# Performance work log

Measured on AMD Instinct MI355X. Metric: run time of the kernel, lower is better.

The kernel has to match this reference:

```python
import jax, jax.numpy as jnp
import numpy as np

B, E, IN, OUT = 512, 8, 1024, 1024


def setup_inputs() -> dict:
    key = jax.random.key(0)
    k1, k2, k3, k4 = jax.random.split(key, 4)
    x = jax.random.normal(k1, (B, IN), dtype=jnp.float32)
    expert_weights = jax.random.uniform(k2, (B, E), dtype=jnp.float32)
    # kaiming_uniform per expert with a=sqrt(5): bound = sqrt(6/((1+a^2)*fan_in)) = 1/sqrt(fan_in)
    wb = 1.0 / np.sqrt(IN)
    weight = jax.random.uniform(k3, (E, OUT, IN), dtype=jnp.float32, minval=-wb, maxval=wb)
    bias = jax.random.uniform(k4, (E, OUT), dtype=jnp.float32, minval=-wb, maxval=wb)
    return {"x": x, "expert_weights": expert_weights, "weight": weight, "bias": bias}


def reference(x, expert_weights, weight, bias):
    # Same math as: blended_W = einsum('bk,koi->boi'); bmm(blended_W, x[...,None]) + blended_b
    # fused as a single contraction to avoid the [B, out, in] intermediate.
    y = jnp.einsum('bk,koi,bi->bo', expert_weights, weight, x)
    b = jnp.einsum('bk,ko->bo', expert_weights, bias)
    return y + b
```

## Files before the change

### kernel.cpp

```cpp
#include <hip/hip_runtime.h>
#include <hip/hip_bf16.h>


#define BDIM 512
#define EDIM 8
#define INDIM 1024
#define OUTDIM 1024
#define NDIM (EDIM * OUTDIM)

typedef __attribute__((ext_vector_type(8))) short frag8;
typedef __attribute__((ext_vector_type(4))) float f32x4;

__device__ inline void async_ld16(void* lds, const void* g) {
  __builtin_amdgcn_global_load_lds(
      (const __attribute__((address_space(1))) void*)g,
      (__attribute__((address_space(3))) void*)lds, 16, 0, 0);
}

__device__ inline ushort f2bf(float f) {
  unsigned u = __builtin_bit_cast(unsigned, f);
  u += 0x7fffu + ((u >> 16) & 1u);
  return (ushort)(u >> 16);
}

__global__ __launch_bounds__(256) void prep_kernel(
    const float* __restrict__ W, const float* __restrict__ x,
    ushort* __restrict__ wsW, ushort* __restrict__ wsX) {
  const int NW = EDIM * OUTDIM * INDIM / 4;
  int i = blockIdx.x * 256 + threadIdx.x;
  const float4* src;
  ushort* dst;
  if (i < NW) {
    src = (const float4*)W + i;
    dst = wsW + (size_t)i * 4;
  } else {
    int j = i - NW;
    src = (const float4*)x + j;
    dst = wsX + (size_t)j * 4;
  }
  float4 v = *src;
  ushort4 o;
  o.x = f2bf(v.x); o.y = f2bf(v.y); o.z = f2bf(v.z); o.w = f2bf(v.w);
  *(ushort4*)dst = o;
}

#define TM 128
#define TN 128
#define BK 64

__global__ __launch_bounds__(256) void gemm_bt(
    const ushort* __restrict__ A,
    const ushort* __restrict__ Bm,
    float* __restrict__ Z) {
  __shared__ __align__(16) ushort As[TM * BK];
  __shared__ __align__(16) ushort Bs[TN * BK];

  const int tid  = threadIdx.x;
  const int lane = tid & 63;
  const int wave = tid >> 6;
  const int n0 = blockIdx.x * TN;
  const int m0 = blockIdx.y * TM;

  const int wr   = (wave >> 1) * 64;
  const int wc   = (wave & 1) * 64;
  const int l15  = lane & 15;
  const int quad = lane >> 4;

  const int srow  = lane >> 3;
  const int selem = (lane & 7) * 8;

  f32x4 acc[4][4] = {};

  for (int k0 = 0; k0 < INDIM; k0 += BK) {
#pragma unroll
    for (int c = 0; c < 4; ++c) {
      const int chunk = wave * 4 + c;
      const int row = chunk * 8 + srow;
      async_ld16(&As[chunk * 512],
                 A + (size_t)(m0 + row) * INDIM + k0 + selem);
      async_ld16(&Bs[chunk * 512],
                 Bm + (size_t)(n0 + row) * INDIM + k0 + selem);
    }
    __syncthreads();

#pragma unroll
    for (int kk = 0; kk < BK; kk += 32) {
      frag8 a[4], b[4];
#pragma unroll
      for (int i = 0; i < 4; ++i) {
        a[i] = *(const frag8*)&As[(wr + i * 16 + l15) * BK + kk + quad * 8];
        b[i] = *(const frag8*)&Bs[(wc + i * 16 + l15) * BK + kk + quad * 8];
      }
#pragma unroll
      for (int i = 0; i < 4; ++i)
#pragma unroll
        for (int j = 0; j < 4; ++j)
          acc[i][j] = __builtin_amdgcn_mfma_f32_16x16x32_bf16(a[i], b[j], acc[i][j], 0, 0, 0);
    }
    __syncthreads();
  }

#pragma unroll
  for (int i = 0; i < 4; ++i) {
    const int mrow = m0 + wr + i * 16 + quad * 4;
#pragma unroll
    for (int j = 0; j < 4; ++j) {
      const int ncol = n0 + wc + j * 16 + l15;
#pragma unroll
      for (int r = 0; r < 4; ++r)
        Z[(size_t)(mrow + r) * NDIM + ncol] = acc[i][j][r];
    }
  }
}

__global__ __launch_bounds__(256) void blend_kernel(
    const float* __restrict__ Z, const float* __restrict__ ew,
    const float* __restrict__ bias, float* __restrict__ out) {
  int idx = blockIdx.x * 256 + threadIdx.x;
  int b = idx >> 10;
  int o = idx & 1023;
  const float* zb = Z + (size_t)b * NDIM + o;
  float y = 0.f;
#pragma unroll
  for (int k = 0; k < EDIM; ++k)
    y += ew[b * EDIM + k] * (zb[k * OUTDIM] + bias[k * OUTDIM + o]);
  out[idx] = y;
}

__global__ __launch_bounds__(256) void fallback_kernel(
    const float* __restrict__ x, const float* __restrict__ ew,
    const float* __restrict__ W, const float* __restrict__ bias,
    float* __restrict__ out) {
  int idx = blockIdx.x * 256 + threadIdx.x;
  int b = idx >> 10;
  int o = idx & 1023;
  float y = 0.f;
  for (int k = 0; k < EDIM; ++k) {
    const float* wr = W + ((size_t)k * OUTDIM + o) * INDIM;
    const float* xr = x + (size_t)b * INDIM;
    float dot = 0.f;
    for (int i = 0; i < INDIM; ++i) dot += wr[i] * xr[i];
    y += ew[b * EDIM + k] * (dot + bias[k * OUTDIM + o]);
  }
  out[idx] = y;
}

extern "C" void kernel_launch(void* const* d_in, const int* in_sizes, int n_in,
                              void* d_out, int out_size, void* d_ws, size_t ws_size,
                              hipStream_t stream) {
  const float* x    = (const float*)d_in[0];
  const float* ew   = (const float*)d_in[1];
  const float* W    = (const float*)d_in[2];
  const float* bias = (const float*)d_in[3];
  float* out = (float*)d_out;

  const size_t offW = 0;
  const size_t offX = (size_t)16 << 20;
  const size_t offZ = (size_t)17 << 20;
  const size_t need = (size_t)33 << 20;

  if (ws_size < need) {
    fallback_kernel<<<2048, 256, 0, stream>>>(x, ew, W, bias, out);
    return;
  }

  char* ws = (char*)d_ws;
  ushort* wsW = (ushort*)(ws + offW);
  ushort* wsX = (ushort*)(ws + offX);
  float*  wsZ = (float*)(ws + offZ);

  prep_kernel<<<8704, 256, 0, stream>>>(W, x, wsW, wsX);
  gemm_bt<<<dim3(64, 4), 256, 0, stream>>>(wsX, wsW, wsZ);
  blend_kernel<<<2048, 256, 0, stream>>>(wsZ, ew, bias, out);
}
```

Measured before the change: 111.6 us.

## Fuse bf16 conversion, expert GEMM and expert blending into one kernel

Replaces the separate weight/input bf16 conversion pass, the GEMM writing an [B, E*OUT] intermediate, and the blend kernel with a single kernel. Each block loads fp32 x and W tiles, converts them to bf16 while staging into padded LDS, runs MFMA over the 8 experts for 16 output columns, and applies bias and expert weights in the epilogue. This removes the bf16 weight copy and the large fp32 intermediate round-trip through memory, and drops two launches. In exchange, W is reread in fp32 by each batch-row block, and the load pipeline is only a register prefetch with one LDS buffer.

```diff
diff --git a/kernel.cpp b/kernel.cpp
--- a/kernel.cpp
+++ b/kernel.cpp
@@ -2,20 +2,17 @@
 #include <hip/hip_bf16.h>
 
 
-#define BDIM 512
 #define EDIM 8
 #define INDIM 1024
 #define OUTDIM 1024
-#define NDIM (EDIM * OUTDIM)
+#define TM 128
+#define ON 16
+#define TN 128
+#define BK 64
+#define LDP 72
 
 typedef __attribute__((ext_vector_type(8))) short frag8;
 typedef __attribute__((ext_vector_type(4))) float f32x4;
-
-__device__ inline void async_ld16(void* lds, const void* g) {
-  __builtin_amdgcn_global_load_lds(
-      (const __attribute__((address_space(1))) void*)g,
-      (__attribute__((address_space(3))) void*)lds, 16, 0, 0);
-}
 
 __device__ inline ushort f2bf(float f) {
   unsigned u = __builtin_bit_cast(unsigned, f);
@@ -23,126 +20,109 @@
   return (ushort)(u >> 16);
 }
 
-__global__ __launch_bounds__(256) void prep_kernel(
-    const float* __restrict__ W, const float* __restrict__ x,
-    ushort* __restrict__ wsW, ushort* __restrict__ wsX) {
-  const int NW = EDIM * OUTDIM * INDIM / 4;
-  int i = blockIdx.x * 256 + threadIdx.x;
-  const float4* src;
-  ushort* dst;
-  if (i < NW) {
-    src = (const float4*)W + i;
-    dst = wsW + (size_t)i * 4;
-  } else {
-    int j = i - NW;
-    src = (const float4*)x + j;
-    dst = wsX + (size_t)j * 4;
-  }
-  float4 v = *src;
+__device__ inline ushort4 f4_to_bf4(float4 v) {
   ushort4 o;
   o.x = f2bf(v.x); o.y = f2bf(v.y); o.z = f2bf(v.z); o.w = f2bf(v.w);
-  *(ushort4*)dst = o;
+  return o;
 }
 
-#define TM 128
-#define TN 128
-#define BK 64
-
-__global__ __launch_bounds__(256) void gemm_bt(
-    const ushort* __restrict__ A,
-    const ushort* __restrict__ Bm,
-    float* __restrict__ Z) {
-  __shared__ __align__(16) ushort As[TM * BK];
-  __shared__ __align__(16) ushort Bs[TN * BK];
+__global__ __launch_bounds__(512) void expert_linear_fused(
+    const float* __restrict__ x,
+    const float* __restrict__ ew,
+    const float* __restrict__ W,
+    const float* __restrict__ bias,
+    float* __restrict__ out) {
+  __shared__ __align__(16) ushort As[TM * LDP];
+  __shared__ __align__(16) ushort Bs[TN * LDP];
 
   const int tid  = threadIdx.x;
   const int lane = tid & 63;
   const int wave = tid >> 6;
-  const int n0 = blockIdx.x * TN;
+  const int o0 = blockIdx.x * ON;
   const int m0 = blockIdx.y * TM;
 
-  const int wr   = (wave >> 1) * 64;
-  const int wc   = (wave & 1) * 64;
   const int l15  = lane & 15;
   const int quad = lane >> 4;
 
-  const int srow  = lane >> 3;
-  const int selem = (lane & 7) * 8;
+  const int slot = tid & 15;
+  const int srow = tid >> 4;
 
-  f32x4 acc[4][4] = {};
+  const float* aptr[4];
+  const float* bptr[4];
+  ushort* awr[4];
+  ushort* bwr[4];
+#pragma unroll
+  for (int p = 0; p < 4; ++p) {
+    const int ar = srow + 32 * p;
+    aptr[p] = x + (size_t)(m0 + ar) * INDIM + slot * 4;
+    awr[p]  = &As[ar * LDP + slot * 4];
+    const int br = srow + 32 * p;
+    const int wrow = (br >> 4) * 1024 + o0 + (br & 15);
+    bptr[p] = W + (size_t)wrow * INDIM + slot * 4;
+    bwr[p]  = &Bs[br * LDP + slot * 4];
+  }
 
-  for (int k0 = 0; k0 < INDIM; k0 += BK) {
+  const ushort* ard = &As[(wave * 16 + l15) * LDP + quad * 8];
+  const ushort* brd[8];
 #pragma unroll
-    for (int c = 0; c < 4; ++c) {
-      const int chunk = wave * 4 + c;
-      const int row = chunk * 8 + srow;
-      async_ld16(&As[chunk * 512],
-                 A + (size_t)(m0 + row) * INDIM + k0 + selem);
-      async_ld16(&Bs[chunk * 512],
-                 Bm + (size_t)(n0 + row) * INDIM + k0 + selem);
+  for (int j = 0; j < 8; ++j)
+    brd[j] = &Bs[(j * 16 + l15) * LDP + quad * 8];
+
+  f32x4 acc[8] = {};
+
+  float4 pa[4], pb[4];
+#pragma unroll
+  for (int p = 0; p < 4; ++p) {
+    pa[p] = *(const float4*)aptr[p];
+    pb[p] = *(const float4*)bptr[p];
+  }
+
+  for (int it = 0; it < INDIM / BK; ++it) {
+#pragma unroll
+    for (int p = 0; p < 4; ++p) {
+      *(ushort4*)awr[p] = f4_to_bf4(pa[p]);
+      *(ushort4*)bwr[p] = f4_to_bf4(pb[p]);
+    }
+    if (it + 1 < INDIM / BK) {
+#pragma unroll
+      for (int p = 0; p < 4; ++p) {
+        aptr[p] += BK; bptr[p] += BK;
+        pa[p] = *(const float4*)aptr[p];
+        pb[p] = *(const float4*)bptr[p];
+      }
     }
     __syncthreads();
 
 #pragma unroll
     for (int kk = 0; kk < BK; kk += 32) {
-      frag8 a[4], b[4];
+      frag8 a = *(const frag8*)(ard + kk);
+      frag8 b[8];
 #pragma unroll
-      for (int i = 0; i < 4; ++i) {
-        a[i] = *(const frag8*)&As[(wr + i * 16 + l15) * BK + kk + quad * 8];
-        b[i] = *(const frag8*)&Bs[(wc + i * 16 + l15) * BK + kk + quad * 8];
-      }
+      for (int j = 0; j < 8; ++j)
+        b[j] = *(const frag8*)(brd[j] + kk);
 #pragma unroll
-      for (int i = 0; i < 4; ++i)
-#pragma unroll
-        for (int j = 0; j < 4; ++j)
-          acc[i][j] = __builtin_amdgcn_mfma_f32_16x16x32_bf16(a[i], b[j], acc[i][j], 0, 0, 0);
+      for (int j = 0; j < 8; ++j)
+        acc[j] = __builtin_amdgcn_mfma_f32_16x16x32_bf16(a, b[j], acc[j], 0, 0, 0);
     }
     __syncthreads();
   }
 
+  const int ocol = o0 + l15;
+  float bgather[8];
 #pragma unroll
-  for (int i = 0; i < 4; ++i) {
-    const int mrow = m0 + wr + i * 16 + quad * 4;
+  for (int j = 0; j < 8; ++j) bgather[j] = bias[j * OUTDIM + ocol];
+
+  const int rbase = m0 + wave * 16 + quad * 4;
 #pragma unroll
-    for (int j = 0; j < 4; ++j) {
-      const int ncol = n0 + wc + j * 16 + l15;
+  for (int r = 0; r < 4; ++r) {
+    const int b = rbase + r;
+    const float* ewb = ew + b * EDIM;
+    float y = 0.f;
 #pragma unroll
-      for (int r = 0; r < 4; ++r)
-        Z[(size_t)(mrow + r) * NDIM + ncol] = acc[i][j][r];
-    }
+    for (int j = 0; j < 8; ++j)
+      y += ewb[j] * (acc[j][r] + bgather[j]);
+    out[(size_t)b * OUTDIM + ocol] = y;
   }
-}
-
-__global__ __launch_bounds__(256) void blend_kernel(
-    const float* __restrict__ Z, const float* __restrict__ ew,
-    const float* __restrict__ bias, float* __restrict__ out) {
-  int idx = blockIdx.x * 256 + threadIdx.x;
-  int b = idx >> 10;
-  int o = idx & 1023;
-  const float* zb = Z + (size_t)b * NDIM + o;
-  float y = 0.f;
-#pragma unroll
-  for (int k = 0; k < EDIM; ++k)
-    y += ew[b * EDIM + k] * (zb[k * OUTDIM] + bias[k * OUTDIM + o]);
-  out[idx] = y;
-}
-
-__global__ __launch_bounds__(256) void fallback_kernel(
-    const float* __restrict__ x, const float* __restrict__ ew,
-    const float* __restrict__ W, const float* __restrict__ bias,
-    float* __restrict__ out) {
-  int idx = blockIdx.x * 256 + threadIdx.x;
-  int b = idx >> 10;
-  int o = idx & 1023;
-  float y = 0.f;
-  for (int k = 0; k < EDIM; ++k) {
-    const float* wr = W + ((size_t)k * OUTDIM + o) * INDIM;
-    const float* xr = x + (size_t)b * INDIM;
-    float dot = 0.f;
-    for (int i = 0; i < INDIM; ++i) dot += wr[i] * xr[i];
-    y += ew[b * EDIM + k] * (dot + bias[k * OUTDIM + o]);
-  }
-  out[idx] = y;
 }
 
 extern "C" void kernel_launch(void* const* d_in, const int* in_sizes, int n_in,
@@ -154,22 +134,6 @@
   const float* bias = (const float*)d_in[3];
   float* out = (float*)d_out;
 
-  const size_t offW = 0;
-  const size_t offX = (size_t)16 << 20;
-  const size_t offZ = (size_t)17 << 20;
-  const size_t need = (size_t)33 << 20;
-
-  if (ws_size < need) {
-    fallback_kernel<<<2048, 256, 0, stream>>>(x, ew, W, bias, out);
-    return;
-  }
-
-  char* ws = (char*)d_ws;
-  ushort* wsW = (ushort*)(ws + offW);
-  ushort* wsX = (ushort*)(ws + offX);
-  float*  wsZ = (float*)(ws + offZ);
-
-  prep_kernel<<<8704, 256, 0, stream>>>(W, x, wsW, wsX);
-  gemm_bt<<<dim3(64, 4), 256, 0, stream>>>(wsX, wsW, wsZ);
-  blend_kernel<<<2048, 256, 0, stream>>>(wsZ, ew, bias, out);
+  expert_linear_fused<<<dim3(OUTDIM / ON, 512 / TM), 512, 0, stream>>>(
+      x, ew, W, bias, out);
 }
```

New measurement: 100.4 us. 10.0% less time.

## Fuse weight conversion and expert blend into a double-buffered GEMM

Applied to the files above, without the earlier changes.

Drops the separate pass that converts the whole fp32 weight tensor to bf16 and the pass that blends the expert outputs. The GEMM now loads fp32 weights directly, converts them in registers and writes them to a double-buffered LDS tile. The expert-weighted sum and bias are applied in the epilogue with a shuffle reduction, so the 16MB Z intermediate is never written. Each block covers 8 outputs across all 8 experts with 256 batch rows. The grid is 128x2 blocks of 512 threads, and W is re-read once per batch tile (twice).

```diff
diff --git a/kernel.cpp b/kernel.cpp
--- a/kernel.cpp
+++ b/kernel.cpp
@@ -2,11 +2,14 @@
 #include <hip/hip_bf16.h>
 
 
-#define BDIM 512
 #define EDIM 8
 #define INDIM 1024
 #define OUTDIM 1024
-#define NDIM (EDIM * OUTDIM)
+#define BATCH 512
+#define TM 256
+#define TNR 64
+#define BK 64
+#define NITER (INDIM / BK)
 
 typedef __attribute__((ext_vector_type(8))) short frag8;
 typedef __attribute__((ext_vector_type(4))) float f32x4;
@@ -23,108 +26,119 @@
   return (ushort)(u >> 16);
 }
 
-__global__ __launch_bounds__(256) void prep_kernel(
-    const float* __restrict__ W, const float* __restrict__ x,
-    ushort* __restrict__ wsW, ushort* __restrict__ wsX) {
-  const int NW = EDIM * OUTDIM * INDIM / 4;
-  int i = blockIdx.x * 256 + threadIdx.x;
-  const float4* src;
-  ushort* dst;
-  if (i < NW) {
-    src = (const float4*)W + i;
-    dst = wsW + (size_t)i * 4;
-  } else {
-    int j = i - NW;
-    src = (const float4*)x + j;
-    dst = wsX + (size_t)j * 4;
-  }
-  float4 v = *src;
+__device__ inline ushort4 f4_to_bf4(float4 v) {
   ushort4 o;
   o.x = f2bf(v.x); o.y = f2bf(v.y); o.z = f2bf(v.z); o.w = f2bf(v.w);
-  *(ushort4*)dst = o;
+  return o;
 }
 
-#define TM 128
-#define TN 128
-#define BK 64
+__global__ __launch_bounds__(256) void prep_x(const float* __restrict__ x,
+                                              ushort* __restrict__ wsX) {
+  int i = blockIdx.x * 256 + threadIdx.x;
+  float4 v = ((const float4*)x)[i];
+  ((ushort4*)wsX)[i] = f4_to_bf4(v);
+}
 
-__global__ __launch_bounds__(256) void gemm_bt(
-    const ushort* __restrict__ A,
-    const ushort* __restrict__ Bm,
-    float* __restrict__ Z) {
-  __shared__ __align__(16) ushort As[TM * BK];
-  __shared__ __align__(16) ushort Bs[TN * BK];
+__global__ __launch_bounds__(512) void gemm_fused(
+    const ushort* __restrict__ Xb,
+    const float* __restrict__ ew,
+    const float* __restrict__ W,
+    const float* __restrict__ bias,
+    float* __restrict__ out) {
+  __shared__ __align__(16) ushort As[2][TM * BK];
+  __shared__ __align__(16) ushort Bs[2][TNR * BK];
 
   const int tid  = threadIdx.x;
   const int lane = tid & 63;
   const int wave = tid >> 6;
-  const int n0 = blockIdx.x * TN;
+  const int o0 = blockIdx.x * 8;
   const int m0 = blockIdx.y * TM;
 
-  const int wr   = (wave >> 1) * 64;
-  const int wc   = (wave & 1) * 64;
   const int l15  = lane & 15;
   const int quad = lane >> 4;
 
-  const int srow  = lane >> 3;
-  const int selem = (lane & 7) * 8;
+  const ushort* aG = Xb + (size_t)(m0 + (lane >> 3)) * INDIM + (lane & 7) * 8;
 
-  f32x4 acc[4][4] = {};
+  int fi0 = tid, fi1 = tid + 512;
+  int r0 = fi0 >> 4, s0 = fi0 & 15;
+  int r1 = fi1 >> 4, s1 = fi1 & 15;
+  const float* bG0 = W + (size_t)((r0 >> 3) * 1024 + o0 + (r0 & 7)) * INDIM + s0 * 4;
+  const float* bG1 = W + (size_t)((r1 >> 3) * 1024 + o0 + (r1 & 7)) * INDIM + s1 * 4;
+  ushort* bW0base = &Bs[0][0] + r0 * BK + s0 * 4;
+  ushort* bW1base = &Bs[0][0] + r1 * BK + s1 * 4;
 
-  for (int k0 = 0; k0 < INDIM; k0 += BK) {
+  f32x4 acc[2][4] = {};
+
 #pragma unroll
-    for (int c = 0; c < 4; ++c) {
-      const int chunk = wave * 4 + c;
-      const int row = chunk * 8 + srow;
-      async_ld16(&As[chunk * 512],
-                 A + (size_t)(m0 + row) * INDIM + k0 + selem);
-      async_ld16(&Bs[chunk * 512],
-                 Bm + (size_t)(n0 + row) * INDIM + k0 + selem);
+  for (int cc = 0; cc < 4; ++cc) {
+    const int c = wave * 4 + cc;
+    async_ld16(&As[0][c * 512], aG + (size_t)c * 8 * INDIM);
+  }
+  {
+    float4 v0 = *(const float4*)bG0;
+    float4 v1 = *(const float4*)bG1;
+    *(ushort4*)bW0base = f4_to_bf4(v0);
+    *(ushort4*)bW1base = f4_to_bf4(v1);
+  }
+  __syncthreads();
+
+  for (int it = 0; it < NITER; ++it) {
+    const int cur = it & 1, nxt = cur ^ 1;
+    const bool more = (it + 1 < NITER);
+    float4 v0, v1;
+    if (more) {
+      const int k0n = (it + 1) * BK;
+#pragma unroll
+      for (int cc = 0; cc < 4; ++cc) {
+        const int c = wave * 4 + cc;
+        async_ld16(&As[nxt][c * 512], aG + (size_t)c * 8 * INDIM + k0n);
+      }
+      v0 = *(const float4*)(bG0 + k0n);
+      v1 = *(const float4*)(bG1 + k0n);
     }
-    __syncthreads();
 
 #pragma unroll
     for (int kk = 0; kk < BK; kk += 32) {
-      frag8 a[4], b[4];
+      frag8 a[2], b[4];
 #pragma unroll
-      for (int i = 0; i < 4; ++i) {
-        a[i] = *(const frag8*)&As[(wr + i * 16 + l15) * BK + kk + quad * 8];
-        b[i] = *(const frag8*)&Bs[(wc + i * 16 + l15) * BK + kk + quad * 8];
-      }
+      for (int i = 0; i < 2; ++i)
+        a[i] = *(const frag8*)&As[cur][(wave * 32 + i * 16 + l15) * BK + kk + quad * 8];
 #pragma unroll
-      for (int i = 0; i < 4; ++i)
+      for (int j = 0; j < 4; ++j)
+        b[j] = *(const frag8*)&Bs[cur][(j * 16 + l15) * BK + kk + quad * 8];
+#pragma unroll
+      for (int i = 0; i < 2; ++i)
 #pragma unroll
         for (int j = 0; j < 4; ++j)
           acc[i][j] = __builtin_amdgcn_mfma_f32_16x16x32_bf16(a[i], b[j], acc[i][j], 0, 0, 0);
     }
+
+    if (more) {
+      *(ushort4*)(bW0base + nxt * (TNR * BK)) = f4_to_bf4(v0);
+      *(ushort4*)(bW1base + nxt * (TNR * BK)) = f4_to_bf4(v1);
+    }
     __syncthreads();
   }
 
+  const int h  = l15 >> 3;
+  const int oc = o0 + (l15 & 7);
+  float bgather[4];
 #pragma unroll
-  for (int i = 0; i < 4; ++i) {
-    const int mrow = m0 + wr + i * 16 + quad * 4;
+  for (int j = 0; j < 4; ++j) bgather[j] = bias[(2 * j + h) * OUTDIM + oc];
+
 #pragma unroll
-    for (int j = 0; j < 4; ++j) {
-      const int ncol = n0 + wc + j * 16 + l15;
+  for (int i = 0; i < 2; ++i) {
 #pragma unroll
-      for (int r = 0; r < 4; ++r)
-        Z[(size_t)(mrow + r) * NDIM + ncol] = acc[i][j][r];
+    for (int r = 0; r < 4; ++r) {
+      const int b = m0 + wave * 32 + i * 16 + quad * 4 + r;
+      float p = 0.f;
+#pragma unroll
+      for (int j = 0; j < 4; ++j)
+        p += ew[b * EDIM + 2 * j + h] * (acc[i][j][r] + bgather[j]);
+      p += __shfl_xor(p, 8, 64);
+      if (h == 0) out[(size_t)b * OUTDIM + oc] = p;
     }
   }
-}
-
-__global__ __launch_bounds__(256) void blend_kernel(
-    const float* __restrict__ Z, const float* __restrict__ ew,
-    const float* __restrict__ bias, float* __restrict__ out) {
-  int idx = blockIdx.x * 256 + threadIdx.x;
-  int b = idx >> 10;
-  int o = idx & 1023;
-  const float* zb = Z + (size_t)b * NDIM + o;
-  float y = 0.f;
-#pragma unroll
-  for (int k = 0; k < EDIM; ++k)
-    y += ew[b * EDIM + k] * (zb[k * OUTDIM] + bias[k * OUTDIM + o]);
-  out[idx] = y;
 }
 
 __global__ __launch_bounds__(256) void fallback_kernel(
@@ -140,7 +154,7 @@
     const float* xr = x + (size_t)b * INDIM;
     float dot = 0.f;
     for (int i = 0; i < INDIM; ++i) dot += wr[i] * xr[i];
-    y += ew[b * EDIM + k] * (dot + bias[k * OUTDIM + o]);
+    y += ew[k + b * EDIM] * (dot + bias[k * OUTDIM + o]);
   }
   out[idx] = y;
 }
@@ -154,22 +168,13 @@
   const float* bias = (const float*)d_in[3];
   float* out = (float*)d_out;
 
-  const size_t offW = 0;
-  const size_t offX = (size_t)16 << 20;
-  const size_t offZ = (size_t)17 << 20;
-  const size_t need = (size_t)33 << 20;
-
-  if (ws_size < need) {
+  if (ws_size < (size_t)(BATCH * INDIM * 2)) {
     fallback_kernel<<<2048, 256, 0, stream>>>(x, ew, W, bias, out);
     return;
   }
+  ushort* wsX = (ushort*)d_ws;
 
-  char* ws = (char*)d_ws;
-  ushort* wsW = (ushort*)(ws + offW);
-  ushort* wsX = (ushort*)(ws + offX);
-  float*  wsZ = (float*)(ws + offZ);
-
-  prep_kernel<<<8704, 256, 0, stream>>>(W, x, wsW, wsX);
-  gemm_bt<<<dim3(64, 4), 256, 0, stream>>>(wsX, wsW, wsZ);
-  blend_kernel<<<2048, 256, 0, stream>>>(wsZ, ew, bias, out);
+  prep_x<<<512, 256, 0, stream>>>(x, wsX);
+  gemm_fused<<<dim3(OUTDIM / 8, BATCH / TM), 512, 0, stream>>>(
+      wsX, ew, W, bias, out);
 }
```

Result: faster. 105.6 us (-5.4%).
